# Performance work log

Hardware: AMD Instinct MI355X
Metric: run time of the kernel (lower is better)

The kernel has to match this reference:

```python
import jax, jax.numpy as jnp
import numpy as np

N = 40000; E = 500000; IN = 128; ED = 16; HID = 64; HEADS = 4; OUT = 256; B = 128
NEG = 0.2  # GATv2 leaky_relu negative slope


def _add_self_loops(edge_index, edge_attr, n):
    # PyG add_self_loops with fill_value='mean': loop attr = mean of incoming edge attrs per node
    dst = edge_index[1]
    s = jax.ops.segment_sum(edge_attr, dst, num_segments=n)
    c = jax.ops.segment_sum(jnp.ones((edge_attr.shape[0],), edge_attr.dtype), dst, num_segments=n)
    loop_attr = s / jnp.maximum(c, 1.0)[:, None]
    loops = jnp.arange(n, dtype=edge_index.dtype)
    ei = jnp.concatenate([edge_index, jnp.stack([loops, loops])], axis=1)
    ea = jnp.concatenate([edge_attr, loop_attr], axis=0)
    return ei, ea


def _seg_softmax(logits, seg, n):
    m = jax.ops.segment_max(logits, seg, num_segments=n)
    m = jnp.where(jnp.isfinite(m), m, 0.0)  # guard empty segments
    e = jnp.exp(logits - m[seg])
    z = jax.ops.segment_sum(e, seg, num_segments=n)
    return e / (z[seg] + 1e-16)


def _gatv2(x, src, dst, ea, Wl, bl, Wr, br, We, att, bias, heads, oc, concat):
    n = x.shape[0]
    xl = (x @ Wl + bl).reshape(n, heads, oc)  # lin_l (source/message transform)
    xr = (x @ Wr + br).reshape(n, heads, oc)  # lin_r (target transform)
    ef = (ea @ We).reshape(-1, heads, oc)     # lin_edge (no bias)
    s = jax.nn.leaky_relu(xl[src] + xr[dst] + ef, NEG)  # [Etot,H,C]
    alpha = _seg_softmax(jnp.einsum('ehc,hc->eh', s, att), dst, n)  # scatter-softmax over dst
    out = jax.ops.segment_sum(xl[src] * alpha[..., None], dst, num_segments=n)  # [N,H,C]
    out = out.reshape(n, heads * oc) if concat else out.mean(axis=1)
    return out + bias


def setup_inputs():
    ks = jax.random.split(jax.random.key(0), 32)
    W = lambda i, shp: jax.random.normal(ks[i], shp, jnp.float32) * 0.05
    z = lambda d: jnp.zeros((d,), jnp.float32)
    H = HEADS * HID
    return dict(
        x=jax.random.normal(ks[0], (N, IN), jnp.float32),
        edge_index=jax.random.randint(ks[1], (2, E), 0, N),
        edge_attr=jax.random.normal(ks[2], (E, ED), jnp.float32),
        batch=jnp.sort(jax.random.randint(ks[3], (N,), 0, B)),
        batch_size=B,
        c1_Wl=W(4, (IN, H)), c1_bl=z(H), c1_Wr=W(5, (IN, H)), c1_br=z(H), c1_We=W(6, (ED, H)), c1_att=W(7, (HEADS, HID)), c1_bias=z(H),
        c2_Wl=W(8, (H, H)), c2_bl=z(H), c2_Wr=W(9, (H, H)), c2_br=z(H), c2_We=W(10, (ED, H)), c2_att=W(11, (HEADS, HID)), c2_bias=z(H),
        c3_Wl=W(12, (H, OUT)), c3_bl=z(OUT), c3_Wr=W(13, (H, OUT)), c3_br=z(OUT), c3_We=W(14, (ED, OUT)), c3_att=W(15, (1, OUT)), c3_bias=z(OUT),
        gate_W1=W(16, (OUT, 128)), gate_b1=z(128), gate_W2=W(17, (128, 1)), gate_b2=z(1),
        reg_W1=W(18, (OUT, 128)), reg_b1=z(128), reg_W2=W(19, (128, 2)), reg_b2=z(2),
    )


def reference(x, edge_index, edge_attr, batch, batch_size,
              c1_Wl, c1_bl, c1_Wr, c1_br, c1_We, c1_att, c1_bias,
              c2_Wl, c2_bl, c2_Wr, c2_br, c2_We, c2_att, c2_bias,
              c3_Wl, c3_bl, c3_Wr, c3_br, c3_We, c3_att, c3_bias,
              gate_W1, gate_b1, gate_W2, gate_b2,
              reg_W1, reg_b1, reg_W2, reg_b2):
    # task_type='homo_lumo' path; dropout disabled (inference)
    ei, ea = _add_self_loops(edge_index, edge_attr, N)
    src, dst = ei[0], ei[1]
    h = jax.nn.relu(_gatv2(x, src, dst, ea, c1_Wl, c1_bl, c1_Wr, c1_br, c1_We, c1_att, c1_bias, HEADS, HID, True))
    h = jax.nn.relu(_gatv2(h, src, dst, ea, c2_Wl, c2_bl, c2_Wr, c2_br, c2_We, c2_att, c2_bias, HEADS, HID, True))
    h = _gatv2(h, src, dst, ea, c3_Wl, c3_bl, c3_Wr, c3_br, c3_We, c3_att, c3_bias, 1, OUT, True)
    # AttentionalAggregation pooling
    gate = jax.nn.relu(h @ gate_W1 + gate_b1) @ gate_W2 + gate_b2  # [N,1]
    a = _seg_softmax(gate[:, 0], batch, batch_size)
    g = jax.ops.segment_sum(h * a[:, None], batch, num_segments=batch_size)  # [B,OUT]
    return jax.nn.relu(g @ reg_W1 + reg_b1) @ reg_W2 + reg_b2  # [B,2]
```

## Files before the change

### kernel.cpp

```cpp
#include <hip/hip_runtime.h>
#include <math.h>

constexpr int N_NODES = 40000;
constexpr int N_EDGES = 500000;
constexpr int ETOT    = N_EDGES + N_NODES;
constexpr int IN_DIM  = 128;
constexpr int ED_DIM  = 16;
constexpr int FEAT    = 256;
constexpr int BATCH   = 128;
constexpr float NEG   = 0.2f;
constexpr int NCHUNK  = (N_NODES + 255) / 256;

__global__ __launch_bounds__(256) void k_deg(const int* __restrict__ dst, int* __restrict__ deg)
{
    int e = blockIdx.x * 256 + threadIdx.x;
    if (e >= ETOT) return;
    int v = e < N_EDGES ? dst[e] : e - N_EDGES;
    atomicAdd(&deg[v], 1);
}

__global__ __launch_bounds__(256) void k_scan1(const int* __restrict__ deg, int* __restrict__ bsum)
{
    __shared__ int s[256];
    int t = threadIdx.x;
    int idx = blockIdx.x * 256 + t;
    s[t] = idx < N_NODES ? deg[idx] : 0;
    __syncthreads();
    for (int st = 128; st; st >>= 1) { if (t < st) s[t] += s[t + st]; __syncthreads(); }
    if (t == 0) bsum[blockIdx.x] = s[0];
}

__global__ __launch_bounds__(256) void k_scan2(const int* __restrict__ bsum,
    int* __restrict__ boff, int* __restrict__ rowptr)
{
    __shared__ int s[256];
    int t = threadIdx.x;
    int v = t < NCHUNK ? bsum[t] : 0;
    s[t] = v;
    __syncthreads();
    for (int off = 1; off < 256; off <<= 1) {
        int x = (t >= off) ? s[t - off] : 0;
        __syncthreads();
        s[t] += x;
        __syncthreads();
    }
    if (t < NCHUNK) boff[t] = s[t] - v;
    if (t == 0) rowptr[N_NODES] = ETOT;
}

__global__ __launch_bounds__(256) void k_scan3(const int* __restrict__ deg,
    const int* __restrict__ boff, int* __restrict__ rowptr)
{
    __shared__ int s[256];
    int t = threadIdx.x;
    int idx = blockIdx.x * 256 + t;
    int v = idx < N_NODES ? deg[idx] : 0;
    s[t] = v;
    __syncthreads();
    for (int off = 1; off < 256; off <<= 1) {
        int x = (t >= off) ? s[t - off] : 0;
        __syncthreads();
        s[t] += x;
        __syncthreads();
    }
    if (idx < N_NODES) rowptr[idx] = boff[blockIdx.x] + s[t] - v;
}

__global__ __launch_bounds__(256) void k_fill(const int* __restrict__ dst,
    const int* __restrict__ rowptr, int* __restrict__ fill, int* __restrict__ elist)
{
    int e = blockIdx.x * 256 + threadIdx.x;
    if (e >= ETOT) return;
    int v = e < N_EDGES ? dst[e] : e - N_EDGES;
    int pos = rowptr[v] + atomicAdd(&fill[v], 1);
    elist[pos] = e;
}

__global__ __launch_bounds__(256) void k_loop_csr(const int* __restrict__ elist,
    const int* __restrict__ rowptr, const float* __restrict__ ea, float* __restrict__ loop_attr)
{
    int t = blockIdx.x * 256 + threadIdx.x;
    if (t >= N_NODES * ED_DIM) return;
    int n = t >> 4, d = t & 15;
    int p0 = rowptr[n], p1 = rowptr[n + 1];
    float s = 0.f; int c = 0;
    for (int p = p0; p < p1; ++p) {
        int e = elist[p];
        if (e < N_EDGES) { s += ea[(size_t)e * ED_DIM + d]; ++c; }
    }
    loop_attr[t] = s / (float)(c > 0 ? c : 1);
}

__global__ __launch_bounds__(256) void k_gemm(const float* __restrict__ A, const float* __restrict__ W,
    const float* __restrict__ bias, float* __restrict__ C, int M, int N, int K, int act)
{
    __shared__ float As[16][68];
    __shared__ float Bs[16][132];
    int t = threadIdx.x;
    int bm = blockIdx.x * 64, bn = blockIdx.y * 128;
    int arow = t >> 2, akc = (t & 3) << 2;
    int bkr = t >> 4, bnc = (t & 15) << 3;
    int tmr = (t >> 4) << 2, tnc = (t & 15) << 3;
    float acc[4][8] = {};
    for (int k0 = 0; k0 < K; k0 += 16) {
        float4 av  = *(const float4*)(A + (size_t)(bm + arow) * K + k0 + akc);
        float4 bv0 = *(const float4*)(W + (size_t)(k0 + bkr) * N + bn + bnc);
        float4 bv1 = *(const float4*)(W + (size_t)(k0 + bkr) * N + bn + bnc + 4);
        As[akc + 0][arow] = av.x; As[akc + 1][arow] = av.y;
        As[akc + 2][arow] = av.z; As[akc + 3][arow] = av.w;
        *(float4*)&Bs[bkr][bnc]     = bv0;
        *(float4*)&Bs[bkr][bnc + 4] = bv1;
        __syncthreads();
        #pragma unroll
        for (int k = 0; k < 16; ++k) {
            float4 a  = *(const float4*)&As[k][tmr];
            float4 b0 = *(const float4*)&Bs[k][tnc];
            float4 b1 = *(const float4*)&Bs[k][tnc + 4];
            float am[4] = {a.x, a.y, a.z, a.w};
            float bnv[8] = {b0.x, b0.y, b0.z, b0.w, b1.x, b1.y, b1.z, b1.w};
            #pragma unroll
            for (int i = 0; i < 4; ++i)
                #pragma unroll
                for (int j = 0; j < 8; ++j)
                    acc[i][j] = fmaf(am[i], bnv[j], acc[i][j]);
        }
        __syncthreads();
    }
    float bb[8];
    #pragma unroll
    for (int j = 0; j < 8; ++j) bb[j] = bias[bn + tnc + j];
    #pragma unroll
    for (int i = 0; i < 4; ++i) {
        float4 o0, o1;
        o0.x = acc[i][0] + bb[0]; o0.y = acc[i][1] + bb[1];
        o0.z = acc[i][2] + bb[2]; o0.w = acc[i][3] + bb[3];
        o1.x = acc[i][4] + bb[4]; o1.y = acc[i][5] + bb[5];
        o1.z = acc[i][6] + bb[6]; o1.w = acc[i][7] + bb[7];
        if (act) {
            o0.x = fmaxf(o0.x, 0.f); o0.y = fmaxf(o0.y, 0.f); o0.z = fmaxf(o0.z, 0.f); o0.w = fmaxf(o0.w, 0.f);
            o1.x = fmaxf(o1.x, 0.f); o1.y = fmaxf(o1.y, 0.f); o1.z = fmaxf(o1.z, 0.f); o1.w = fmaxf(o1.w, 0.f);
        }
        *(float4*)(C + (size_t)(bm + tmr + i) * N + bn + tnc)     = o0;
        *(float4*)(C + (size_t)(bm + tmr + i) * N + bn + tnc + 4) = o1;
    }
}

static void launch_gemm(const float* A, const float* W, const float* bias, float* C,
                        int M, int N, int K, int act, hipStream_t stream)
{
    dim3 grid(M / 64, N / 128);
    k_gemm<<<grid, 256, 0, stream>>>(A, W, bias, C, M, N, K, act);
}


#define RESOLVE_SRC(s) do {                                                           \
    int e_ = eS[s];                                                                   \
    int real_ = e_ < N_EDGES;                                                         \
    srcS[s] = real_ ? srcArr[real_ ? e_ : 0] : (e_ - N_EDGES);                        \
} while (0)

#define XELOAD(s) do {                                                                \
    int e_ = eS[s];                                                                   \
    int real_ = e_ < N_EDGES;                                                         \
    const float4* eb4_ = reinterpret_cast<const float4*>(                             \
        real_ ? ea + (size_t)e_ * ED_DIM                                              \
              : loop_attr + (size_t)(e_ - N_EDGES) * ED_DIM);                         \
    evS[s][0] = eb4_[0]; evS[s][1] = eb4_[1];                                         \
    evS[s][2] = eb4_[2]; evS[s][3] = eb4_[3];                                         \
    const float* xp_ = xl + (size_t)srcS[s] * FEAT + base;                            \
    xlvS[s][0] = xp_[0]; xlvS[s][1] = xp_[16];                                        \
    xlvS[s][2] = xp_[32]; xlvS[s][3] = xp_[48];                                       \
} while (0)

#define COMPUTE(s) do {                                                               \
    float ef0_ = 0.f, ef1_ = 0.f, ef2_ = 0.f, ef3_ = 0.f;                             \
    const float* ed_ = (const float*)evS[s];                                          \
    _Pragma("unroll")                                                                 \
    for (int d_ = 0; d_ < ED_DIM; ++d_) {                                             \
        float a_ = ed_[d_];                                                           \
        ef0_ = fmaf(a_, weR[d_][0], ef0_); ef1_ = fmaf(a_, weR[d_][1], ef1_);         \
        ef2_ = fmaf(a_, weR[d_][2], ef2_); ef3_ = fmaf(a_, weR[d_][3], ef3_);         \
    }                                                                                 \
    float s0_ = xlvS[s][0] + xrv[0] + ef0_;                                           \
    float s1_ = xlvS[s][1] + xrv[1] + ef1_;                                           \
    float s2_ = xlvS[s][2] + xrv[2] + ef2_;                                           \
    float s3_ = xlvS[s][3] + xrv[3] + ef3_;                                           \
    s0_ = fmaxf(s0_, 0.f) + NEG * fminf(s0_, 0.f);                                    \
    s1_ = fmaxf(s1_, 0.f) + NEG * fminf(s1_, 0.f);                                    \
    s2_ = fmaxf(s2_, 0.f) + NEG * fminf(s2_, 0.f);                                    \
    s3_ = fmaxf(s3_, 0.f) + NEG * fminf(s3_, 0.f);                                    \
    float l_ = fmaf(s0_, attR[0], fmaf(s1_, attR[1], fmaf(s2_, attR[2], s3_ * attR[3])));\
    l_ += __shfl_xor(l_, 1, 64);                                                      \
    l_ += __shfl_xor(l_, 2, 64);                                                      \
    l_ += __shfl_xor(l_, 4, 64);                                                      \
    l_ += __shfl_xor(l_, 8, 64);                                                      \
    if (H == 1) { l_ += __shfl_xor(l_, 16, 64); l_ += __shfl_xor(l_, 32, 64); }       \
    float nm_ = fmaxf(m, l_);                                                         \
    float sc_ = __expf(m - nm_);                                                      \
    float w_  = __expf(l_ - nm_);                                                     \
    z = fmaf(z, sc_, w_);                                                             \
    m = nm_;                                                                          \
    acc[0] = fmaf(acc[0], sc_, w_ * xlvS[s][0]);                                      \
    acc[1] = fmaf(acc[1], sc_, w_ * xlvS[s][1]);                                      \
    acc[2] = fmaf(acc[2], sc_, w_ * xlvS[s][2]);                                      \
    acc[3] = fmaf(acc[3], sc_, w_ * xlvS[s][3]);                                      \
} while (0)

#define STEP(i0, i1, i2) do {                                                         \
    int pn_ = p + 3; pn_ = pn_ > pe ? pe : pn_;                                       \
    eS[i0] = elist[pn_];                                                              \
    RESOLVE_SRC(i2);                                                                  \
    XELOAD(i1);                                                                       \
    COMPUTE(i0);                                                                      \
} while (0)

template <int H, int RELU>
__global__ __launch_bounds__(256, 3) void k_gat(
    const float* __restrict__ xl, const float* __restrict__ xr,
    const float* __restrict__ ea, const float* __restrict__ loop_attr,
    const int* __restrict__ srcArr, const int* __restrict__ elist, const int* __restrict__ rowptr,
    const float* __restrict__ We, const float* __restrict__ att,
    const float* __restrict__ bias, float* __restrict__ out)
{
    int t = threadIdx.x;
    int lane = t & 63;
    int n = __builtin_amdgcn_readfirstlane(blockIdx.x * 4 + (t >> 6));
    int q = lane >> 4;
    int u = lane & 15;
    int base = q * 64 + u;

    float weR[ED_DIM][4];
    #pragma unroll
    for (int d = 0; d < ED_DIM; ++d) {
        #pragma unroll
        for (int j = 0; j < 4; ++j) weR[d][j] = We[d * FEAT + base + 16 * j];
    }
    float attR[4], xrv[4];
    #pragma unroll
    for (int j = 0; j < 4; ++j) {
        attR[j] = att[base + 16 * j];
        xrv[j]  = xr[(size_t)n * FEAT + base + 16 * j];
    }

    float m = -INFINITY, z = 0.f;
    float acc[4] = {0.f, 0.f, 0.f, 0.f};

    int p0 = rowptr[n], p1 = rowptr[n + 1];
    int pe = p1 - 1;

    int eS[3], srcS[3];
    float4 evS[3][4];
    float  xlvS[3][4];

    eS[0] = elist[p0];
    { int p1c = p0 + 1 > pe ? pe : p0 + 1; eS[1] = elist[p1c]; }
    { int p2c = p0 + 2 > pe ? pe : p0 + 2; eS[2] = elist[p2c]; }
    RESOLVE_SRC(0);
    RESOLVE_SRC(1);
    XELOAD(0);

    int p = p0;
    while (true) {
        STEP(0, 1, 2); if (++p >= p1) break;
        STEP(1, 2, 0); if (++p >= p1) break;
        STEP(2, 0, 1); if (++p >= p1) break;
    }

    float inv = 1.0f / (z + 1e-16f);
    #pragma unroll
    for (int j = 0; j < 4; ++j) {
        float o = fmaf(acc[j], inv, bias[base + 16 * j]);
        if (RELU) o = fmaxf(o, 0.f);
        out[(size_t)n * FEAT + base + 16 * j] = o;
    }
}

__global__ __launch_bounds__(256) void k_gate_score(const float* __restrict__ ghid,
    const float* __restrict__ W2, const float* __restrict__ b2, float* __restrict__ gate)
{
    int lane = threadIdx.x & 63;
    int n = blockIdx.x * 4 + (threadIdx.x >> 6);
    float v = ghid[(size_t)n * 128 + lane] * W2[lane] + ghid[(size_t)n * 128 + lane + 64] * W2[lane + 64];
    #pragma unroll
    for (int off = 32; off > 0; off >>= 1) v += __shfl_xor(v, off, 64);
    if (lane == 0) gate[n] = v + b2[0];
}

__device__ __forceinline__ int lbound(const int* a, int n, int v)
{
    int lo = 0, hi = n;
    while (lo < hi) { int mid = (lo + hi) >> 1; if (a[mid] < v) lo = mid + 1; else hi = mid; }
    return lo;
}

__global__ __launch_bounds__(256) void k_pool(const float* __restrict__ gate,
    const float* __restrict__ h, const int* __restrict__ batch, float* __restrict__ g)
{
    int b = blockIdx.x;
    int t = threadIdx.x;
    __shared__ float red[256];
    int start = lbound(batch, N_NODES, b);
    int end   = lbound(batch, N_NODES, b + 1);

    float mx = -INFINITY;
    for (int n = start + t; n < end; n += 256) mx = fmaxf(mx, gate[n]);
    red[t] = mx; __syncthreads();
    for (int s = 128; s; s >>= 1) { if (t < s) red[t] = fmaxf(red[t], red[t + s]); __syncthreads(); }
    float m = red[0];
    __syncthreads();

    float zs = 0.f;
    for (int n = start + t; n < end; n += 256) zs += __expf(gate[n] - m);
    red[t] = zs; __syncthreads();
    for (int s = 128; s; s >>= 1) { if (t < s) red[t] += red[t + s]; __syncthreads(); }
    float z = red[0];

    float gs = 0.f;
    for (int n = start; n < end; ++n) gs += __expf(gate[n] - m) * h[(size_t)n * FEAT + t];
    g[b * FEAT + t] = gs / (z + 1e-16f);
}

__global__ __launch_bounds__(128) void k_reg(const float* __restrict__ g,
    const float* __restrict__ W1, const float* __restrict__ b1,
    const float* __restrict__ W2, const float* __restrict__ b2, float* __restrict__ out)
{
    int b = blockIdx.x, t = threadIdx.x;
    __shared__ float sg[FEAT];
    sg[t] = g[b * FEAT + t];
    sg[t + 128] = g[b * FEAT + t + 128];
    __syncthreads();
    float hv = b1[t];
    for (int k = 0; k < FEAT; ++k) hv += sg[k] * W1[k * 128 + t];
    hv = fmaxf(hv, 0.f);
    __shared__ float p0s[128], p1s[128];
    p0s[t] = hv * W2[t * 2 + 0];
    p1s[t] = hv * W2[t * 2 + 1];
    __syncthreads();
    for (int s = 64; s; s >>= 1) {
        if (t < s) { p0s[t] += p0s[t + s]; p1s[t] += p1s[t + s]; }
        __syncthreads();
    }
    if (t == 0) { out[b * 2 + 0] = p0s[0] + b2[0]; out[b * 2 + 1] = p1s[0] + b2[1]; }
}

extern "C" void kernel_launch(void* const* d_in, const int* in_sizes, int n_in,
                              void* d_out, int out_size, void* d_ws, size_t ws_size,
                              hipStream_t stream)
{
    const float* x       = (const float*)d_in[0];
    const int*   ei      = (const int*)d_in[1];
    const float* ea      = (const float*)d_in[2];
    const int*   batch   = (const int*)d_in[3];
    const float* c1_Wl   = (const float*)d_in[5];
    const float* c1_bl   = (const float*)d_in[6];
    const float* c1_Wr   = (const float*)d_in[7];
    const float* c1_br   = (const float*)d_in[8];
    const float* c1_We   = (const float*)d_in[9];
    const float* c1_att  = (const float*)d_in[10];
    const float* c1_bias = (const float*)d_in[11];
    const float* c2_Wl   = (const float*)d_in[12];
    const float* c2_bl   = (const float*)d_in[13];
    const float* c2_Wr   = (const float*)d_in[14];
    const float* c2_br   = (const float*)d_in[15];
    const float* c2_We   = (const float*)d_in[16];
    const float* c2_att  = (const float*)d_in[17];
    const float* c2_bias = (const float*)d_in[18];
    const float* c3_Wl   = (const float*)d_in[19];
    const float* c3_bl   = (const float*)d_in[20];
    const float* c3_Wr   = (const float*)d_in[21];
    const float* c3_br   = (const float*)d_in[22];
    const float* c3_We   = (const float*)d_in[23];
    const float* c3_att  = (const float*)d_in[24];
    const float* c3_bias = (const float*)d_in[25];
    const float* gate_W1 = (const float*)d_in[26];
    const float* gate_b1 = (const float*)d_in[27];
    const float* gate_W2 = (const float*)d_in[28];
    const float* gate_b2 = (const float*)d_in[29];
    const float* reg_W1  = (const float*)d_in[30];
    const float* reg_b1  = (const float*)d_in[31];
    const float* reg_W2  = (const float*)d_in[32];
    const float* reg_b2  = (const float*)d_in[33];

    const int* srcArr = ei;
    const int* dstArr = ei + N_EDGES;

    float* ws = (float*)d_ws;
    size_t off = 0;
    auto alloc = [&](size_t nf) { float* p = ws + off; off += (nf + 63) & ~(size_t)63; return p; };
    float* xl        = alloc((size_t)N_NODES * FEAT);
    float* xr        = alloc((size_t)N_NODES * FEAT);
    float* h         = alloc((size_t)N_NODES * FEAT);
    float* loop_attr = alloc((size_t)N_NODES * ED_DIM);
    float* gpool     = alloc((size_t)BATCH * FEAT);
    int* ibase  = (int*)(ws + off);
    int* deg    = ibase;
    int* fill   = ibase + N_NODES;
    int* rowptr = ibase + 2 * N_NODES;
    int* bsum   = ibase + 3 * N_NODES + 64;
    int* boff   = bsum + 256;
    int* elist  = boff + 256;

    float* ghid = xl;
    float* gate = xr;

    hipMemsetAsync(deg, 0, (size_t)2 * N_NODES * sizeof(int), stream);

    k_deg<<<(ETOT + 255) / 256, 256, 0, stream>>>(dstArr, deg);
    k_scan1<<<NCHUNK, 256, 0, stream>>>(deg, bsum);
    k_scan2<<<1, 256, 0, stream>>>(bsum, boff, rowptr);
    k_scan3<<<NCHUNK, 256, 0, stream>>>(deg, boff, rowptr);
    k_fill<<<(ETOT + 255) / 256, 256, 0, stream>>>(dstArr, rowptr, fill, elist);
    k_loop_csr<<<(N_NODES * ED_DIM + 255) / 256, 256, 0, stream>>>(elist, rowptr, ea, loop_attr);

    launch_gemm(x, c1_Wl, c1_bl, xl, N_NODES, FEAT, IN_DIM, 0, stream);
    launch_gemm(x, c1_Wr, c1_br, xr, N_NODES, FEAT, IN_DIM, 0, stream);
    k_gat<4, 1><<<N_NODES / 4, 256, 0, stream>>>(xl, xr, ea, loop_attr, srcArr, elist, rowptr,
                                                 c1_We, c1_att, c1_bias, h);
    launch_gemm(h, c2_Wl, c2_bl, xl, N_NODES, FEAT, FEAT, 0, stream);
    launch_gemm(h, c2_Wr, c2_br, xr, N_NODES, FEAT, FEAT, 0, stream);
    k_gat<4, 1><<<N_NODES / 4, 256, 0, stream>>>(xl, xr, ea, loop_attr, srcArr, elist, rowptr,
                                                 c2_We, c2_att, c2_bias, h);
    launch_gemm(h, c3_Wl, c3_bl, xl, N_NODES, FEAT, FEAT, 0, stream);
    launch_gemm(h, c3_Wr, c3_br, xr, N_NODES, FEAT, FEAT, 0, stream);
    k_gat<1, 0><<<N_NODES / 4, 256, 0, stream>>>(xl, xr, ea, loop_attr, srcArr, elist, rowptr,
                                                 c3_We, c3_att, c3_bias, h);

    launch_gemm(h, gate_W1, gate_b1, ghid, N_NODES, 128, FEAT, 1, stream);
    k_gate_score<<<N_NODES / 4, 256, 0, stream>>>(ghid, gate_W2, gate_b2, gate);
    k_pool<<<BATCH, 256, 0, stream>>>(gate, h, batch, gpool);
    k_reg<<<BATCH, 128, 0, stream>>>(gpool, reg_W1, reg_b1, reg_W2, reg_b2, (float*)d_out);
}
```

Baseline: 1.228 ms.

## Store src with edge id in CSR, enlarge GEMM tile, shorten GAT prefetch pipeline

The CSR edge list now stores (src, edge id) pairs, so the GAT kernel no longer does a dependent srcArr lookup per edge. The software pipeline drops from three stages to two. The GEMM moves from 64x128 to 128x128 tiles with 8x8 per-thread accumulators and gains row bounds guards, raising arithmetic intensity at the cost of more registers and fewer blocks. An empty asm pins the edge-weight registers in VGPRs.

```diff
diff --git a/kernel.cpp b/kernel.cpp
--- a/kernel.cpp
+++ b/kernel.cpp
@@ -66,17 +66,18 @@
     if (idx < N_NODES) rowptr[idx] = boff[blockIdx.x] + s[t] - v;
 }
 
-__global__ __launch_bounds__(256) void k_fill(const int* __restrict__ dst,
-    const int* __restrict__ rowptr, int* __restrict__ fill, int* __restrict__ elist)
+__global__ __launch_bounds__(256) void k_fill(const int* __restrict__ srcA, const int* __restrict__ dst,
+    const int* __restrict__ rowptr, int* __restrict__ fill, int2* __restrict__ elist2)
 {
     int e = blockIdx.x * 256 + threadIdx.x;
     if (e >= ETOT) return;
-    int v = e < N_EDGES ? dst[e] : e - N_EDGES;
+    int v = e < N_EDGES ? dst[e]  : e - N_EDGES;
+    int s = e < N_EDGES ? srcA[e] : e - N_EDGES;
     int pos = rowptr[v] + atomicAdd(&fill[v], 1);
-    elist[pos] = e;
-}
-
-__global__ __launch_bounds__(256) void k_loop_csr(const int* __restrict__ elist,
+    elist2[pos] = make_int2(s, e);
+}
+
+__global__ __launch_bounds__(256) void k_loop_csr(const int2* __restrict__ elist2,
     const int* __restrict__ rowptr, const float* __restrict__ ea, float* __restrict__ loop_attr)
 {
     int t = blockIdx.x * 256 + threadIdx.x;
@@ -85,7 +86,7 @@
     int p0 = rowptr[n], p1 = rowptr[n + 1];
     float s = 0.f; int c = 0;
     for (int p = p0; p < p1; ++p) {
-        int e = elist[p];
+        int e = elist2[p].y;
         if (e < N_EDGES) { s += ea[(size_t)e * ED_DIM + d]; ++c; }
     }
     loop_attr[t] = s / (float)(c > 0 ? c : 1);
@@ -94,43 +95,57 @@
 __global__ __launch_bounds__(256) void k_gemm(const float* __restrict__ A, const float* __restrict__ W,
     const float* __restrict__ bias, float* __restrict__ C, int M, int N, int K, int act)
 {
-    __shared__ float As[16][68];
-    __shared__ float Bs[16][132];
-    int t = threadIdx.x;
-    int bm = blockIdx.x * 64, bn = blockIdx.y * 128;
-    int arow = t >> 2, akc = (t & 3) << 2;
-    int bkr = t >> 4, bnc = (t & 15) << 3;
-    int tmr = (t >> 4) << 2, tnc = (t & 15) << 3;
-    float acc[4][8] = {};
+    __shared__ float As[16][136];
+    __shared__ float Bs[16][136];
+    int t = threadIdx.x;
+    int bm = blockIdx.x * 128, bn = blockIdx.y * 128;
+    int tr = t >> 4, tc = t & 15;
+    int mr0 = tr * 8, nc0 = tc * 4;
+
+    float acc[8][8] = {};
+
     for (int k0 = 0; k0 < K; k0 += 16) {
-        float4 av  = *(const float4*)(A + (size_t)(bm + arow) * K + k0 + akc);
-        float4 bv0 = *(const float4*)(W + (size_t)(k0 + bkr) * N + bn + bnc);
-        float4 bv1 = *(const float4*)(W + (size_t)(k0 + bkr) * N + bn + bnc + 4);
-        As[akc + 0][arow] = av.x; As[akc + 1][arow] = av.y;
-        As[akc + 2][arow] = av.z; As[akc + 3][arow] = av.w;
-        *(float4*)&Bs[bkr][bnc]     = bv0;
-        *(float4*)&Bs[bkr][bnc + 4] = bv1;
+        #pragma unroll
+        for (int ii = 0; ii < 2; ++ii) {
+            int i = t + ii * 256;
+            int row = i >> 2, kq = (i & 3) << 2;
+            int r = bm + row; r = r < M ? r : M - 1;
+            float4 av = *(const float4*)(A + (size_t)r * K + k0 + kq);
+            As[kq + 0][row] = av.x; As[kq + 1][row] = av.y;
+            As[kq + 2][row] = av.z; As[kq + 3][row] = av.w;
+        }
+        #pragma unroll
+        for (int ii = 0; ii < 2; ++ii) {
+            int i = t + ii * 256;
+            int krow = i >> 5, nq = (i & 31) << 2;
+            float4 bv = *(const float4*)(W + (size_t)(k0 + krow) * N + bn + nq);
+            *(float4*)&Bs[krow][nq] = bv;
+        }
         __syncthreads();
         #pragma unroll
         for (int k = 0; k < 16; ++k) {
-            float4 a  = *(const float4*)&As[k][tmr];
-            float4 b0 = *(const float4*)&Bs[k][tnc];
-            float4 b1 = *(const float4*)&Bs[k][tnc + 4];
-            float am[4] = {a.x, a.y, a.z, a.w};
-            float bnv[8] = {b0.x, b0.y, b0.z, b0.w, b1.x, b1.y, b1.z, b1.w};
+            float4 a0 = *(const float4*)&As[k][mr0];
+            float4 a1 = *(const float4*)&As[k][mr0 + 4];
+            float4 b0 = *(const float4*)&Bs[k][nc0];
+            float4 b1 = *(const float4*)&Bs[k][64 + nc0];
+            float am[8] = {a0.x, a0.y, a0.z, a0.w, a1.x, a1.y, a1.z, a1.w};
+            float bv[8] = {b0.x, b0.y, b0.z, b0.w, b1.x, b1.y, b1.z, b1.w};
             #pragma unroll
-            for (int i = 0; i < 4; ++i)
+            for (int i = 0; i < 8; ++i)
                 #pragma unroll
                 for (int j = 0; j < 8; ++j)
-                    acc[i][j] = fmaf(am[i], bnv[j], acc[i][j]);
+                    acc[i][j] = fmaf(am[i], bv[j], acc[i][j]);
         }
         __syncthreads();
     }
+
     float bb[8];
     #pragma unroll
-    for (int j = 0; j < 8; ++j) bb[j] = bias[bn + tnc + j];
-    #pragma unroll
-    for (int i = 0; i < 4; ++i) {
+    for (int j = 0; j < 4; ++j) { bb[j] = bias[bn + nc0 + j]; bb[j + 4] = bias[bn + 64 + nc0 + j]; }
+    #pragma unroll
+    for (int i = 0; i < 8; ++i) {
+        int row = bm + mr0 + i;
+        if (row >= M) break;
         float4 o0, o1;
         o0.x = acc[i][0] + bb[0]; o0.y = acc[i][1] + bb[1];
         o0.z = acc[i][2] + bb[2]; o0.w = acc[i][3] + bb[3];
@@ -140,35 +155,28 @@
             o0.x = fmaxf(o0.x, 0.f); o0.y = fmaxf(o0.y, 0.f); o0.z = fmaxf(o0.z, 0.f); o0.w = fmaxf(o0.w, 0.f);
             o1.x = fmaxf(o1.x, 0.f); o1.y = fmaxf(o1.y, 0.f); o1.z = fmaxf(o1.z, 0.f); o1.w = fmaxf(o1.w, 0.f);
         }
-        *(float4*)(C + (size_t)(bm + tmr + i) * N + bn + tnc)     = o0;
-        *(float4*)(C + (size_t)(bm + tmr + i) * N + bn + tnc + 4) = o1;
+        *(float4*)(C + (size_t)row * N + bn + nc0)      = o0;
+        *(float4*)(C + (size_t)row * N + bn + 64 + nc0) = o1;
     }
 }
 
 static void launch_gemm(const float* A, const float* W, const float* bias, float* C,
                         int M, int N, int K, int act, hipStream_t stream)
 {
-    dim3 grid(M / 64, N / 128);
+    dim3 grid((M + 127) / 128, N / 128);
     k_gemm<<<grid, 256, 0, stream>>>(A, W, bias, C, M, N, K, act);
 }
 
 
-#define RESOLVE_SRC(s) do {                                                           \
-    int e_ = eS[s];                                                                   \
-    int real_ = e_ < N_EDGES;                                                         \
-    srcS[s] = real_ ? srcArr[real_ ? e_ : 0] : (e_ - N_EDGES);                        \
-} while (0)
-
 #define XELOAD(s) do {                                                                \
-    int e_ = eS[s];                                                                   \
-    int real_ = e_ < N_EDGES;                                                         \
+    int src_ = eS[s].x, e_ = eS[s].y;                                                 \
     const float4* eb4_ = reinterpret_cast<const float4*>(                             \
-        real_ ? ea + (size_t)e_ * ED_DIM                                              \
-              : loop_attr + (size_t)(e_ - N_EDGES) * ED_DIM);                         \
+        (e_ < N_EDGES) ? ea + (size_t)e_ * ED_DIM                                     \
+                       : loop_attr + (size_t)src_ * ED_DIM);                          \
     evS[s][0] = eb4_[0]; evS[s][1] = eb4_[1];                                         \
     evS[s][2] = eb4_[2]; evS[s][3] = eb4_[3];                                         \
-    const float* xp_ = xl + (size_t)srcS[s] * FEAT + base;                            \
-    xlvS[s][0] = xp_[0]; xlvS[s][1] = xp_[16];                                        \
+    const float* xp_ = xl + (size_t)src_ * FEAT + base;                               \
+    xlvS[s][0] = xp_[0];  xlvS[s][1] = xp_[16];                                       \
     xlvS[s][2] = xp_[32]; xlvS[s][3] = xp_[48];                                       \
 } while (0)
 
@@ -206,19 +214,11 @@
     acc[3] = fmaf(acc[3], sc_, w_ * xlvS[s][3]);                                      \
 } while (0)
 
-#define STEP(i0, i1, i2) do {                                                         \
-    int pn_ = p + 3; pn_ = pn_ > pe ? pe : pn_;                                       \
-    eS[i0] = elist[pn_];                                                              \
-    RESOLVE_SRC(i2);                                                                  \
-    XELOAD(i1);                                                                       \
-    COMPUTE(i0);                                                                      \
-} while (0)
-
 template <int H, int RELU>
 __global__ __launch_bounds__(256, 3) void k_gat(
     const float* __restrict__ xl, const float* __restrict__ xr,
     const float* __restrict__ ea, const float* __restrict__ loop_attr,
-    const int* __restrict__ srcArr, const int* __restrict__ elist, const int* __restrict__ rowptr,
+    const int2* __restrict__ elist2, const int* __restrict__ rowptr,
     const float* __restrict__ We, const float* __restrict__ att,
     const float* __restrict__ bias, float* __restrict__ out)
 {
@@ -235,6 +235,12 @@
         #pragma unroll
         for (int j = 0; j < 4; ++j) weR[d][j] = We[d * FEAT + base + 16 * j];
     }
+    #pragma unroll
+    for (int d = 0; d < ED_DIM; ++d) {
+        #pragma unroll
+        for (int j = 0; j < 4; ++j) asm volatile("" : "+v"(weR[d][j]));
+    }
+
     float attR[4], xrv[4];
     #pragma unroll
     for (int j = 0; j < 4; ++j) {
@@ -248,22 +254,24 @@
     int p0 = rowptr[n], p1 = rowptr[n + 1];
     int pe = p1 - 1;
 
-    int eS[3], srcS[3];
-    float4 evS[3][4];
-    float  xlvS[3][4];
-
-    eS[0] = elist[p0];
-    { int p1c = p0 + 1 > pe ? pe : p0 + 1; eS[1] = elist[p1c]; }
-    { int p2c = p0 + 2 > pe ? pe : p0 + 2; eS[2] = elist[p2c]; }
-    RESOLVE_SRC(0);
-    RESOLVE_SRC(1);
+    int2   eS[2];
+    float4 evS[2][4];
+    float  xlvS[2][4];
+
+    eS[0] = elist2[p0];
+    { int pc = p0 + 1 > pe ? pe : p0 + 1; eS[1] = elist2[pc]; }
     XELOAD(0);
 
     int p = p0;
     while (true) {
-        STEP(0, 1, 2); if (++p >= p1) break;
-        STEP(1, 2, 0); if (++p >= p1) break;
-        STEP(2, 0, 1); if (++p >= p1) break;
+        XELOAD(1);
+        { int pn = p + 2 > pe ? pe : p + 2; eS[0] = elist2[pn]; }
+        COMPUTE(0);
+        if (++p >= p1) break;
+        XELOAD(0);
+        { int pn = p + 2 > pe ? pe : p + 2; eS[1] = elist2[pn]; }
+        COMPUTE(1);
+        if (++p >= p1) break;
     }
 
     float inv = 1.0f / (z + 1e-16f);
@@ -398,7 +406,7 @@
     int* rowptr = ibase + 2 * N_NODES;
     int* bsum   = ibase + 3 * N_NODES + 64;
     int* boff   = bsum + 256;
-    int* elist  = boff + 256;
+    int2* elist2 = (int2*)(boff + 256);
 
     float* ghid = xl;
     float* gate = xr;
@@ -409,20 +417,20 @@
     k_scan1<<<NCHUNK, 256, 0, stream>>>(deg, bsum);
     k_scan2<<<1, 256, 0, stream>>>(bsum, boff, rowptr);
     k_scan3<<<NCHUNK, 256, 0, stream>>>(deg, boff, rowptr);
-    k_fill<<<(ETOT + 255) / 256, 256, 0, stream>>>(dstArr, rowptr, fill, elist);
-    k_loop_csr<<<(N_NODES * ED_DIM + 255) / 256, 256, 0, stream>>>(elist, rowptr, ea, loop_attr);
+    k_fill<<<(ETOT + 255) / 256, 256, 0, stream>>>(srcArr, dstArr, rowptr, fill, elist2);
+    k_loop_csr<<<(N_NODES * ED_DIM + 255) / 256, 256, 0, stream>>>(elist2, rowptr, ea, loop_attr);
 
     launch_gemm(x, c1_Wl, c1_bl, xl, N_NODES, FEAT, IN_DIM, 0, stream);
     launch_gemm(x, c1_Wr, c1_br, xr, N_NODES, FEAT, IN_DIM, 0, stream);
-    k_gat<4, 1><<<N_NODES / 4, 256, 0, stream>>>(xl, xr, ea, loop_attr, srcArr, elist, rowptr,
+    k_gat<4, 1><<<N_NODES / 4, 256, 0, stream>>>(xl, xr, ea, loop_attr, elist2, rowptr,
                                                  c1_We, c1_att, c1_bias, h);
     launch_gemm(h, c2_Wl, c2_bl, xl, N_NODES, FEAT, FEAT, 0, stream);
     launch_gemm(h, c2_Wr, c2_br, xr, N_NODES, FEAT, FEAT, 0, stream);
-    k_gat<4, 1><<<N_NODES / 4, 256, 0, stream>>>(xl, xr, ea, loop_attr, srcArr, elist, rowptr,
+    k_gat<4, 1><<<N_NODES / 4, 256, 0, stream>>>(xl, xr, ea, loop_attr, elist2, rowptr,
                                                  c2_We, c2_att, c2_bias, h);
     launch_gemm(h, c3_Wl, c3_bl, xl, N_NODES, FEAT, FEAT, 0, stream);
     launch_gemm(h, c3_Wr, c3_br, xr, N_NODES, FEAT, FEAT, 0, stream);
-    k_gat<1, 0><<<N_NODES / 4, 256, 0, stream>>>(xl, xr, ea, loop_attr, srcArr, elist, rowptr,
+    k_gat<1, 0><<<N_NODES / 4, 256, 0, stream>>>(xl, xr, ea, loop_attr, elist2, rowptr,
                                                  c3_We, c3_att, c3_bias, h);
 
     launch_gemm(h, gate_W1, gate_b1, ghid, N_NODES, 128, FEAT, 1, stream);
```

After: 1.216 ms. About the same (-1.0%).
